# Optimization experiments

Measured on AMD Instinct MI355X. Metric: run time of the kernel, lower is better.

The kernel has to match this reference:

```python
import jax, jax.numpy as jnp
import numpy as np

S_LEN, T_LEN, BATCH, HID = 32, 32, 64, 512


def setup_inputs() -> dict:
    key = jax.random.key(0)
    ks = jax.random.split(key, 5)
    H = HID
    sc = lambda n: 1.0 / np.sqrt(n)
    return {
        "source": jax.random.normal(ks[0], (S_LEN, BATCH, H), jnp.float32),
        "target": jax.random.normal(ks[1], (T_LEN, BATCH, H), jnp.float32),
        # H2h Dense: concat(s_h, t_h) [B, 2H] -> [B, H], linear
        "W_H2h": (jax.random.normal(ks[2], (2 * H, H), jnp.float32) * sc(2 * H)),
        "b_H2h": jnp.zeros((H,), jnp.float32),
        # shared LSTMCell weights (Keras gate order i, f, g, o)
        "W_kernel": (jax.random.normal(ks[3], (H, 4 * H), jnp.float32) * sc(H)),
        "W_rec": (jax.random.normal(ks[4], (H, 4 * H), jnp.float32) * sc(H)),
        "b_lstm": jnp.zeros((4 * H,), jnp.float32),
    }


def _lstm_cell(x, h, c, Wk, Wr, b):
    # Keras LSTMCell math, gate order i, f, g(candidate), o
    z = x @ Wk + h @ Wr + b  # [B, 4H]
    i, f, g, o = jnp.split(z, 4, axis=-1)
    c2 = jax.nn.sigmoid(f) * c + jax.nn.sigmoid(i) * jnp.tanh(g)
    h2 = jax.nn.sigmoid(o) * jnp.tanh(c2)
    return h2, c2


def reference(source, target, W_H2h, b_H2h, W_kernel, W_rec, b_lstm):
    # source: [S, B, H] (time-major), target: [T, B, H]
    T, B, H = target.shape

    def inner(s_state, t_slice):
        # s_state carried along the target axis; t_slice is target cell j state
        s_step, s_h, s_m = s_state
        t_step, t_h, t_m = t_slice
        hmid = jnp.concatenate([s_h, t_h], axis=1) @ W_H2h + b_H2h  # [B, H]
        ns_h, ns_m = _lstm_cell(s_step, hmid, s_m, W_kernel, W_rec, b_lstm)
        nt_h, nt_m = _lstm_cell(t_step, hmid, t_m, W_kernel, W_rec, b_lstm)
        # step arrays get overwritten with the new hidden state
        return (ns_h, ns_h, ns_m), (nt_h, nt_h, nt_m)

    def outer(t_arrays, s_in):
        # fresh source state per outer step i: step = source[i], h = m = 0
        z = jnp.zeros_like(s_in)
        (s_step_f, _, _), t_new = jax.lax.scan(inner, (s_in, z, z), t_arrays)
        return t_new, s_step_f

    zeros = jnp.zeros((T, B, H), source.dtype)
    t_final, source_out = jax.lax.scan(outer, (target, zeros, zeros), source)
    return source_out, t_final[0]
```

## Files before the change

### kernel.cpp

```cpp
#include <hip/hip_runtime.h>

#define BLK 256

typedef __bf16 bf16;
typedef __bf16 bf16x8 __attribute__((ext_vector_type(8)));
typedef float f32x4 __attribute__((ext_vector_type(4)));

__device__ __forceinline__ float sigm(float x) { return 1.f / (1.f + __expf(-x)); }
__device__ __forceinline__ float tanh_(float x) {
    x = fminf(fmaxf(x, -15.f), 15.f);
    float e = __expf(2.f * x);
    return (e - 1.f) / (e + 1.f);
}

__device__ __forceinline__ void gl2lds(const bf16* g, bf16* l) {
    __builtin_amdgcn_global_load_lds((const __attribute__((address_space(1))) void*)g,
                                     (__attribute__((address_space(3))) void*)l, 16, 0, 0);
}

__global__ __launch_bounds__(256) void k_prep(
    const float* __restrict__ src, const float* __restrict__ tgt,
    const float* __restrict__ WH, const float* __restrict__ bH,
    const float* __restrict__ Wk, const float* __restrict__ Wr,
    const float* __restrict__ bl,
    bf16* __restrict__ srcb, bf16* __restrict__ tgtb,
    bf16* __restrict__ WHhi, bf16* __restrict__ WHlo,
    bf16* __restrict__ Wrhi, bf16* __restrict__ Wrlo,
    bf16* __restrict__ P2, float* __restrict__ bz) {
    __shared__ float tile[64][65];
    const int bid = blockIdx.x, t = threadIdx.x;
    if (bid < 512) {
        const float* in = (bid < 256) ? Wr : Wk;
        bf16* ohi = (bid < 256) ? Wrhi : P2;
        bf16* olo = (bid < 256) ? Wrlo : nullptr;
        const int b = bid & 255;
        const int tr = b >> 5, tc = b & 31;
#pragma unroll
        for (int q = 0; q < 16; q++) {
            int idx = q * 256 + t, lr = idx >> 6, lc = idx & 63;
            tile[lr][lc] = in[(size_t)(tr * 64 + lr) * 2048 + tc * 64 + lc];
        }
        __syncthreads();
#pragma unroll
        for (int q = 0; q < 16; q++) {
            int idx = q * 256 + t, lr = idx >> 6, lc = idx & 63;
            float v = tile[lc][lr];
            size_t o = (size_t)(tc * 64 + lr) * 512 + tr * 64 + lc;
            bf16 h = (bf16)v;
            ohi[o] = h;
            if (olo) olo[o] = (bf16)(v - (float)h);
        }
    } else if (bid < 520) {
        int c = (bid - 512) * 256 + t;
        float s = bl[c];
        for (int k = 0; k < 512; k++) s += bH[k] * Wr[(size_t)k * 2048 + c];
        bz[c] = s;
    } else {
        const int gt = (bid - 520) * 256 + t, NT = 504 * 256;
        for (int id = gt; id < 1048576; id += NT) srcb[id] = (bf16)src[id];
        for (int id = gt; id < 1048576; id += NT) tgtb[id] = (bf16)tgt[id];
        for (int id = gt; id < 524288; id += NT) {
            float v = WH[id];
            bf16 h = (bf16)v;
            WHhi[id] = h;
            WHlo[id] = (bf16)(v - (float)h);
        }
    }
}

__global__ __launch_bounds__(256, 4) void k_gemmP(
    const bf16* __restrict__ Wrhi, const bf16* __restrict__ Wrlo,
    const bf16* __restrict__ WHhi, const bf16* __restrict__ WHlo,
    bf16* __restrict__ P3, bf16* __restrict__ P4) {
    __shared__ __align__(16) bf16 At[64 * 64];
    __shared__ __align__(16) bf16 Bt[128 * 64];
    const int t = threadIdx.x, w = t >> 6, l = t & 63;
    const int m0 = (blockIdx.x >> 3) * 64, n0 = (blockIdx.x & 7) * 128;
    f32x4 acc[2][4] = {};
    const bf16* Aps[3] = {Wrhi, Wrlo, Wrhi};
    const bf16* Bps[3] = {WHhi, WHhi, WHlo};
    for (int ph = 0; ph < 3; ph++) {
        const bf16* Ap = Aps[ph] + (size_t)m0 * 512;
        const bf16* Bp = Bps[ph] + (size_t)n0 * 512;
        for (int kt = 0; kt < 8; kt++) {
            int k0 = kt * 64;
            __syncthreads();
#pragma unroll
            for (int q = 0; q < 2; q++) {
                int pp = q * 256 + t;
                int r = pp >> 3, c = (pp & 7) ^ (r & 7);
                gl2lds(Ap + (size_t)r * 512 + k0 + c * 8, &At[(q * 256 + w * 64) * 8]);
            }
#pragma unroll
            for (int q = 0; q < 4; q++) {
                int pp = q * 256 + t;
                int r = pp >> 3, c = (pp & 7) ^ (r & 7);
                gl2lds(Bp + (size_t)r * 512 + k0 + c * 8, &Bt[(q * 256 + w * 64) * 8]);
            }
            __syncthreads();
#pragma unroll
            for (int ks = 0; ks < 2; ks++) {
                int c = ks * 4 + (l >> 4);
                bf16x8 af[2], bb[4];
#pragma unroll
                for (int mt = 0; mt < 2; mt++) {
                    int r = (w >> 1) * 32 + mt * 16 + (l & 15);
                    af[mt] = *(const bf16x8*)&At[(r * 8 + (c ^ (r & 7))) * 8];
                }
#pragma unroll
                for (int g = 0; g < 4; g++) {
                    int r = g * 32 + (w & 1) * 16 + (l & 15);
                    bb[g] = *(const bf16x8*)&Bt[(r * 8 + (c ^ (r & 7))) * 8];
                }
#pragma unroll
                for (int mt = 0; mt < 2; mt++)
#pragma unroll
                    for (int g = 0; g < 4; g++)
                        acc[mt][g] = __builtin_amdgcn_mfma_f32_16x16x32_bf16(
                            af[mt], bb[g], acc[mt][g], 0, 0, 0);
            }
        }
    }
    const bool hihalf = (n0 >= 512);
#pragma unroll
    for (int mt = 0; mt < 2; mt++) {
#pragma unroll
        for (int g = 0; g < 4; g++) {
            int np = n0 + g * 32 + (w & 1) * 16 + (l & 15);
#pragma unroll
            for (int r = 0; r < 4; r++) {
                int c = m0 + (w >> 1) * 32 + mt * 16 + ((l >> 4) << 2) + r;
                float v = acc[mt][g][r];
                if (!hihalf) P4[(size_t)c * 512 + np] = (bf16)v;
                else P3[(size_t)c * 512 + (np - 512)] = (bf16)v;
            }
        }
    }
}

__global__ __launch_bounds__(256, 2) void k_diag4(
    int d, int i_lo,
    const bf16* __restrict__ srcb, const bf16* __restrict__ tgtb,
    const bf16* __restrict__ P2, const bf16* __restrict__ P3,
    const bf16* __restrict__ P4,
    const float* __restrict__ bz,
    const bf16* __restrict__ shR, bf16* __restrict__ shW,
    const bf16* __restrict__ thR, bf16* __restrict__ thW,
    float* __restrict__ sc, float* __restrict__ tc,
    float* __restrict__ out) {
    __shared__ __align__(16) bf16 As[64 * 64];
    __shared__ __align__(16) bf16 At2[64 * 64];
    __shared__ __align__(16) bf16 Bk[128 * 64];
    __shared__ __align__(16) bf16 Bs[128 * 64];
    __shared__ __align__(16) bf16 Bt[128 * 64];
    const int t = threadIdx.x, w = t >> 6, l = t & 63;
    const int cell = blockIdx.x >> 4, ch0 = (blockIdx.x & 15) << 5;
    const int i = i_lo + cell, j = d - i;
    const size_t stI = (size_t)i * 32768, stJ = (size_t)j * 32768;

    const bf16* Asrc = (j == 0 ? srcb : shR) + stI;
    const bf16* Atsrc = (i == 0 ? tgtb : thR) + stJ;
    const bool uS = (j > 0);
    const bool uT = (i > 0);

    f32x4 accS[2][4] = {};
    f32x4 accT[2][4] = {};
    f32x4 accU[2][4] = {};

#pragma unroll 1
    for (int kt = 0; kt < 8; kt++) {
        int k0 = kt * 64;
        __syncthreads();
#pragma unroll
        for (int q = 0; q < 2; q++) {
            int pp = q * 256 + t;
            int r = pp >> 3, c = (pp & 7) ^ (r & 7);
            gl2lds(Asrc + (size_t)r * 512 + k0 + c * 8, &As[(q * 256 + w * 64) * 8]);
        }
#pragma unroll
        for (int q = 0; q < 2; q++) {
            int pp = q * 256 + t;
            int r = pp >> 3, c = (pp & 7) ^ (r & 7);
            gl2lds(Atsrc + (size_t)r * 512 + k0 + c * 8, &At2[(q * 256 + w * 64) * 8]);
        }
#pragma unroll
        for (int q = 0; q < 4; q++) {
            int pp = q * 256 + t;
            int r = pp >> 3, c = (pp & 7) ^ (r & 7);
            size_t grow = (size_t)((r >> 5) * 512 + ch0 + (r & 31));
            gl2lds(P2 + grow * 512 + k0 + c * 8, &Bk[(q * 256 + w * 64) * 8]);
        }
        if (uS) {
#pragma unroll
            for (int q = 0; q < 4; q++) {
                int pp = q * 256 + t;
                int r = pp >> 3, c = (pp & 7) ^ (r & 7);
                size_t grow = (size_t)((r >> 5) * 512 + ch0 + (r & 31));
                gl2lds(P4 + grow * 512 + k0 + c * 8, &Bs[(q * 256 + w * 64) * 8]);
            }
        }
        if (uT) {
#pragma unroll
            for (int q = 0; q < 4; q++) {
                int pp = q * 256 + t;
                int r = pp >> 3, c = (pp & 7) ^ (r & 7);
                size_t grow = (size_t)((r >> 5) * 512 + ch0 + (r & 31));
                gl2lds(P3 + grow * 512 + k0 + c * 8, &Bt[(q * 256 + w * 64) * 8]);
            }
        }
        __syncthreads();
#pragma unroll
        for (int ks = 0; ks < 2; ks++) {
            int cq = ks * 4 + (l >> 4);
            bf16x8 aS[2], aT[2], bb[4];
#pragma unroll
            for (int mt = 0; mt < 2; mt++) {
                int r = (w >> 1) * 32 + mt * 16 + (l & 15);
                int cc = (r * 8 + (cq ^ (r & 7))) * 8;
                aS[mt] = *(const bf16x8*)&As[cc];
                aT[mt] = *(const bf16x8*)&At2[cc];
            }
#pragma unroll
            for (int g = 0; g < 4; g++) {
                int r = g * 32 + (w & 1) * 16 + (l & 15);
                bb[g] = *(const bf16x8*)&Bk[(r * 8 + (cq ^ (r & 7))) * 8];
            }
#pragma unroll
            for (int mt = 0; mt < 2; mt++)
#pragma unroll
                for (int g = 0; g < 4; g++) {
                    accS[mt][g] = __builtin_amdgcn_mfma_f32_16x16x32_bf16(
                        aS[mt], bb[g], accS[mt][g], 0, 0, 0);
                    accT[mt][g] = __builtin_amdgcn_mfma_f32_16x16x32_bf16(
                        aT[mt], bb[g], accT[mt][g], 0, 0, 0);
                }
            if (uS) {
#pragma unroll
                for (int g = 0; g < 4; g++) {
                    int r = g * 32 + (w & 1) * 16 + (l & 15);
                    bb[g] = *(const bf16x8*)&Bs[(r * 8 + (cq ^ (r & 7))) * 8];
                }
#pragma unroll
                for (int mt = 0; mt < 2; mt++)
#pragma unroll
                    for (int g = 0; g < 4; g++)
                        accU[mt][g] = __builtin_amdgcn_mfma_f32_16x16x32_bf16(
                            aS[mt], bb[g], accU[mt][g], 0, 0, 0);
            }
            if (uT) {
#pragma unroll
                for (int g = 0; g < 4; g++) {
                    int r = g * 32 + (w & 1) * 16 + (l & 15);
                    bb[g] = *(const bf16x8*)&Bt[(r * 8 + (cq ^ (r & 7))) * 8];
                }
#pragma unroll
                for (int mt = 0; mt < 2; mt++)
#pragma unroll
                    for (int g = 0; g < 4; g++)
                        accU[mt][g] = __builtin_amdgcn_mfma_f32_16x16x32_bf16(
                            aT[mt], bb[g], accU[mt][g], 0, 0, 0);
            }
        }
    }

    const int h = ch0 + (w & 1) * 16 + (l & 15);
    float bzv[4];
#pragma unroll
    for (int g = 0; g < 4; g++) bzv[g] = bz[g * 512 + h];
#pragma unroll
    for (int mt = 0; mt < 2; mt++) {
#pragma unroll
        for (int r = 0; r < 4; r++) {
            int b = (w >> 1) * 32 + mt * 16 + ((l >> 4) << 2) + r;
            float u0 = accU[mt][0][r], u1 = accU[mt][1][r];
            float u2 = accU[mt][2][r], u3 = accU[mt][3][r];
            {
                float zi = accS[mt][0][r] + u0 + bzv[0];
                float zf = accS[mt][1][r] + u1 + bzv[1];
                float zg = accS[mt][2][r] + u2 + bzv[2];
                float zo = accS[mt][3][r] + u3 + bzv[3];
                size_t off = stI + (size_t)b * 512 + h;
                float cold = uS ? sc[off] : 0.f;
                float c2 = sigm(zf) * cold + sigm(zi) * tanh_(zg);
                float h2 = sigm(zo) * tanh_(c2);
                sc[off] = c2;
                shW[off] = (bf16)h2;
                if (j == 31) out[off] = h2;
            }
            {
                float zi = accT[mt][0][r] + u0 + bzv[0];
                float zf = accT[mt][1][r] + u1 + bzv[1];
                float zg = accT[mt][2][r] + u2 + bzv[2];
                float zo = accT[mt][3][r] + u3 + bzv[3];
                size_t off = stJ + (size_t)b * 512 + h;
                float cold = uT ? tc[off] : 0.f;
                float c2 = sigm(zf) * cold + sigm(zi) * tanh_(zg);
                float h2 = sigm(zo) * tanh_(c2);
                tc[off] = c2;
                thW[off] = (bf16)h2;
                if (i == 31) out[1048576 + off] = h2;
            }
        }
    }
}


extern "C" void kernel_launch(void* const* d_in, const int* in_sizes, int n_in,
                              void* d_out, int out_size, void* d_ws, size_t ws_size,
                              hipStream_t stream) {
    char* w = (char*)d_ws;
    const size_t MB = 1u << 20;
    const float* src = (const float*)d_in[0];
    const float* tgt = (const float*)d_in[1];
    const float* WH = (const float*)d_in[2];
    const float* bH = (const float*)d_in[3];
    const float* Wk = (const float*)d_in[4];
    const float* Wr = (const float*)d_in[5];
    const float* bl = (const float*)d_in[6];
    float* out = (float*)d_out;

    bf16* srcb = (bf16*)(w + 0 * MB);
    bf16* tgtb = (bf16*)(w + 2 * MB);
    bf16* WHhi = (bf16*)(w + 4 * MB);
    bf16* WHlo = (bf16*)(w + 5 * MB);
    bf16* Wrhi = (bf16*)(w + 6 * MB);
    bf16* Wrlo = (bf16*)(w + 8 * MB);
    bf16* P2 = (bf16*)(w + 12 * MB);
    bf16* P3 = (bf16*)(w + 14 * MB);
    bf16* P4 = (bf16*)(w + 16 * MB);
    float* bz = (float*)(w + 20 * MB);
    bf16* sh = (bf16*)(w + 21 * MB);
    bf16* th = (bf16*)(w + 25 * MB);
    float* sc = (float*)(w + 29 * MB);
    float* tc = (float*)(w + 33 * MB);

    k_prep<<<1024, BLK, 0, stream>>>(src, tgt, WH, bH, Wk, Wr, bl, srcb, tgtb,
                                     WHhi, WHlo, Wrhi, Wrlo, P2, bz);
    k_gemmP<<<256, BLK, 0, stream>>>(Wrhi, Wrlo, WHhi, WHlo, P3, P4);

    for (int d = 0; d < 63; d++) {
        int i_lo = d > 31 ? d - 31 : 0;
        int i_hi = d < 31 ? d : 31;
        int Kd = i_hi - i_lo + 1;
        const bf16* shR = sh + (size_t)(d & 1) * 1048576;
        bf16* shW = sh + (size_t)((d + 1) & 1) * 1048576;
        const bf16* thR = th + (size_t)(d & 1) * 1048576;
        bf16* thW = th + (size_t)((d + 1) & 1) * 1048576;
        k_diag4<<<Kd * 16, BLK, 0, stream>>>(d, i_lo, srcb, tgtb, P2, P3, P4,
                                             bz, shR, shW, thR, thW, sc, tc, out);
    }
}
```

Before: 1.460 ms.

## Pair two wavefront cells per 512-thread block with double-buffered LDS staging

```diff
diff --git a/kernel.cpp b/kernel.cpp
--- a/kernel.cpp
+++ b/kernel.cpp
@@ -138,8 +138,8 @@
     }
 }
 
-__global__ __launch_bounds__(256, 2) void k_diag4(
-    int d, int i_lo,
+__global__ __launch_bounds__(512, 2) void k_diag5(
+    int d, int i_lo, int Kd,
     const bf16* __restrict__ srcb, const bf16* __restrict__ tgtb,
     const bf16* __restrict__ P2, const bf16* __restrict__ P3,
     const bf16* __restrict__ P4,
@@ -148,82 +148,69 @@
     const bf16* __restrict__ thR, bf16* __restrict__ thW,
     float* __restrict__ sc, float* __restrict__ tc,
     float* __restrict__ out) {
-    __shared__ __align__(16) bf16 As[64 * 64];
-    __shared__ __align__(16) bf16 At2[64 * 64];
-    __shared__ __align__(16) bf16 Bk[128 * 64];
-    __shared__ __align__(16) bf16 Bs[128 * 64];
-    __shared__ __align__(16) bf16 Bt[128 * 64];
+    __shared__ __align__(16) bf16 AL[2][4 * 4096];
+    __shared__ __align__(16) bf16 BL[2][3 * 8192];
     const int t = threadIdx.x, w = t >> 6, l = t & 63;
-    const int cell = blockIdx.x >> 4, ch0 = (blockIdx.x & 15) << 5;
-    const int i = i_lo + cell, j = d - i;
+    const int q = w >> 2, ww = w & 3;
+    const int pair = blockIdx.x >> 4, ch0 = (blockIdx.x & 15) << 5;
+    const int cell0 = pair * 2;
+    const bool valid = (cell0 + q) < Kd;
+    const int myCell = valid ? cell0 + q : cell0;
+    const int i = i_lo + myCell, j = d - i;
+    const bool uS = (j > 0), uT = (i > 0);
     const size_t stI = (size_t)i * 32768, stJ = (size_t)j * 32768;
 
-    const bf16* Asrc = (j == 0 ? srcb : shR) + stI;
-    const bf16* Atsrc = (i == 0 ? tgtb : thR) + stJ;
-    const bool uS = (j > 0);
-    const bool uT = (i > 0);
+    const int c1 = (cell0 + 1 < Kd) ? cell0 + 1 : cell0;
+    const int i0 = i_lo + cell0, j0 = d - i0;
+    const int i1 = i_lo + c1, j1 = d - i1;
+    const bf16* A0s = (j0 == 0 ? srcb : shR) + (size_t)i0 * 32768;
+    const bf16* A0t = (i0 == 0 ? tgtb : thR) + (size_t)j0 * 32768;
+    const bf16* A1s = (j1 == 0 ? srcb : shR) + (size_t)i1 * 32768;
+    const bf16* A1t = (i1 == 0 ? tgtb : thR) + (size_t)j1 * 32768;
 
     f32x4 accS[2][4] = {};
     f32x4 accT[2][4] = {};
     f32x4 accU[2][4] = {};
 
-#pragma unroll 1
-    for (int kt = 0; kt < 8; kt++) {
-        int k0 = kt * 64;
-        __syncthreads();
-#pragma unroll
-        for (int q = 0; q < 2; q++) {
-            int pp = q * 256 + t;
-            int r = pp >> 3, c = (pp & 7) ^ (r & 7);
-            gl2lds(Asrc + (size_t)r * 512 + k0 + c * 8, &As[(q * 256 + w * 64) * 8]);
-        }
-#pragma unroll
-        for (int q = 0; q < 2; q++) {
-            int pp = q * 256 + t;
-            int r = pp >> 3, c = (pp & 7) ^ (r & 7);
-            gl2lds(Atsrc + (size_t)r * 512 + k0 + c * 8, &At2[(q * 256 + w * 64) * 8]);
-        }
-#pragma unroll
-        for (int q = 0; q < 4; q++) {
-            int pp = q * 256 + t;
+    auto STAGE = [&](int bf, int k0) {
+        bf16* Ab = &AL[bf][0];
+        {
+            int r = t >> 3, c = (t & 7) ^ (r & 7);
+            size_t so = (size_t)r * 512 + k0 + c * 8;
+            gl2lds(A0s + so, Ab + (0 * 512 + w * 64) * 8);
+            gl2lds(A0t + so, Ab + (1 * 512 + w * 64) * 8);
+            gl2lds(A1s + so, Ab + (2 * 512 + w * 64) * 8);
+            gl2lds(A1t + so, Ab + (3 * 512 + w * 64) * 8);
+        }
+        bf16* Bb = &BL[bf][0];
+#pragma unroll
+        for (int qq = 0; qq < 6; qq++) {
+            int pp = (qq & 1) * 512 + t;
             int r = pp >> 3, c = (pp & 7) ^ (r & 7);
             size_t grow = (size_t)((r >> 5) * 512 + ch0 + (r & 31));
-            gl2lds(P2 + grow * 512 + k0 + c * 8, &Bk[(q * 256 + w * 64) * 8]);
-        }
-        if (uS) {
-#pragma unroll
-            for (int q = 0; q < 4; q++) {
-                int pp = q * 256 + t;
-                int r = pp >> 3, c = (pp & 7) ^ (r & 7);
-                size_t grow = (size_t)((r >> 5) * 512 + ch0 + (r & 31));
-                gl2lds(P4 + grow * 512 + k0 + c * 8, &Bs[(q * 256 + w * 64) * 8]);
-            }
-        }
-        if (uT) {
-#pragma unroll
-            for (int q = 0; q < 4; q++) {
-                int pp = q * 256 + t;
-                int r = pp >> 3, c = (pp & 7) ^ (r & 7);
-                size_t grow = (size_t)((r >> 5) * 512 + ch0 + (r & 31));
-                gl2lds(P3 + grow * 512 + k0 + c * 8, &Bt[(q * 256 + w * 64) * 8]);
-            }
-        }
-        __syncthreads();
+            const bf16* M = (qq < 2) ? P2 : (qq < 4) ? P4 : P3;
+            gl2lds(M + grow * 512 + k0 + c * 8, Bb + (qq * 512 + w * 64) * 8);
+        }
+    };
+
+    auto COMPUTE = [&](int bf) {
+        const bf16* Ab = &AL[bf][0];
+        const bf16* Bb = &BL[bf][0];
 #pragma unroll
         for (int ks = 0; ks < 2; ks++) {
             int cq = ks * 4 + (l >> 4);
             bf16x8 aS[2], aT[2], bb[4];
 #pragma unroll
             for (int mt = 0; mt < 2; mt++) {
-                int r = (w >> 1) * 32 + mt * 16 + (l & 15);
-                int cc = (r * 8 + (cq ^ (r & 7))) * 8;
-                aS[mt] = *(const bf16x8*)&As[cc];
-                aT[mt] = *(const bf16x8*)&At2[cc];
+                int r = (ww >> 1) * 32 + mt * 16 + (l & 15);
+                int co = (r * 8 + (cq ^ (r & 7))) * 8;
+                aS[mt] = *(const bf16x8*)&Ab[(q * 2) * 4096 + co];
+                aT[mt] = *(const bf16x8*)&Ab[(q * 2 + 1) * 4096 + co];
             }
 #pragma unroll
             for (int g = 0; g < 4; g++) {
-                int r = g * 32 + (w & 1) * 16 + (l & 15);
-                bb[g] = *(const bf16x8*)&Bk[(r * 8 + (cq ^ (r & 7))) * 8];
+                int r = g * 32 + (ww & 1) * 16 + (l & 15);
+                bb[g] = *(const bf16x8*)&Bb[(r * 8 + (cq ^ (r & 7))) * 8];
             }
 #pragma unroll
             for (int mt = 0; mt < 2; mt++)
@@ -237,8 +224,8 @@
             if (uS) {
 #pragma unroll
                 for (int g = 0; g < 4; g++) {
-                    int r = g * 32 + (w & 1) * 16 + (l & 15);
-                    bb[g] = *(const bf16x8*)&Bs[(r * 8 + (cq ^ (r & 7))) * 8];
+                    int r = g * 32 + (ww & 1) * 16 + (l & 15);
+                    bb[g] = *(const bf16x8*)&Bb[8192 + (r * 8 + (cq ^ (r & 7))) * 8];
                 }
 #pragma unroll
                 for (int mt = 0; mt < 2; mt++)
@@ -250,8 +237,8 @@
             if (uT) {
 #pragma unroll
                 for (int g = 0; g < 4; g++) {
-                    int r = g * 32 + (w & 1) * 16 + (l & 15);
-                    bb[g] = *(const bf16x8*)&Bt[(r * 8 + (cq ^ (r & 7))) * 8];
+                    int r = g * 32 + (ww & 1) * 16 + (l & 15);
+                    bb[g] = *(const bf16x8*)&Bb[16384 + (r * 8 + (cq ^ (r & 7))) * 8];
                 }
 #pragma unroll
                 for (int mt = 0; mt < 2; mt++)
@@ -261,9 +248,22 @@
                             aT[mt], bb[g], accU[mt][g], 0, 0, 0);
             }
         }
-    }
-
-    const int h = ch0 + (w & 1) * 16 + (l & 15);
+    };
+
+    STAGE(0, 0);
+    __syncthreads();
+    int bf = 0;
+#pragma unroll 1
+    for (int kt = 0; kt < 8; kt++) {
+        if (kt < 7) STAGE(bf ^ 1, (kt + 1) * 64);
+        COMPUTE(bf);
+        __syncthreads();
+        bf ^= 1;
+    }
+
+    if (!valid) return;
+
+    const int h = ch0 + (ww & 1) * 16 + (l & 15);
     float bzv[4];
 #pragma unroll
     for (int g = 0; g < 4; g++) bzv[g] = bz[g * 512 + h];
@@ -271,7 +271,7 @@
     for (int mt = 0; mt < 2; mt++) {
 #pragma unroll
         for (int r = 0; r < 4; r++) {
-            int b = (w >> 1) * 32 + mt * 16 + ((l >> 4) << 2) + r;
+            int b = (ww >> 1) * 32 + mt * 16 + ((l >> 4) << 2) + r;
             float u0 = accU[mt][0][r], u1 = accU[mt][1][r];
             float u2 = accU[mt][2][r], u3 = accU[mt][3][r];
             {
@@ -342,11 +342,12 @@
         int i_lo = d > 31 ? d - 31 : 0;
         int i_hi = d < 31 ? d : 31;
         int Kd = i_hi - i_lo + 1;
+        int nPairs = (Kd + 1) >> 1;
         const bf16* shR = sh + (size_t)(d & 1) * 1048576;
         bf16* shW = sh + (size_t)((d + 1) & 1) * 1048576;
         const bf16* thR = th + (size_t)(d & 1) * 1048576;
         bf16* thW = th + (size_t)((d + 1) & 1) * 1048576;
-        k_diag4<<<Kd * 16, BLK, 0, stream>>>(d, i_lo, srcb, tgtb, P2, P3, P4,
-                                             bz, shR, shW, thR, thW, sc, tc, out);
-    }
-}
+        k_diag5<<<nPairs * 16, 512, 0, stream>>>(d, i_lo, Kd, srcb, tgtb, P2, P3, P4,
+                                                 bz, shR, shW, thR, thW, sc, tc, out);
+    }
+}
```

Measured after the change: 1.705 ms. +16.7%, slower.

## Fold kernel weights into recurrent products and split diagonal cells by side

Applied to the files above, without the earlier changes.

```diff
diff --git a/kernel.cpp b/kernel.cpp
--- a/kernel.cpp
+++ b/kernel.cpp
@@ -71,7 +71,9 @@
 __global__ __launch_bounds__(256, 4) void k_gemmP(
     const bf16* __restrict__ Wrhi, const bf16* __restrict__ Wrlo,
     const bf16* __restrict__ WHhi, const bf16* __restrict__ WHlo,
-    bf16* __restrict__ P3, bf16* __restrict__ P4) {
+    const float* __restrict__ Wk,
+    bf16* __restrict__ P1, bf16* __restrict__ P3,
+    bf16* __restrict__ P4, bf16* __restrict__ P5) {
     __shared__ __align__(16) bf16 At[64 * 64];
     __shared__ __align__(16) bf16 Bt[128 * 64];
     const int t = threadIdx.x, w = t >> 6, l = t & 63;
@@ -131,123 +133,84 @@
             for (int r = 0; r < 4; r++) {
                 int c = m0 + (w >> 1) * 32 + mt * 16 + ((l >> 4) << 2) + r;
                 float v = acc[mt][g][r];
-                if (!hihalf) P4[(size_t)c * 512 + np] = (bf16)v;
-                else P3[(size_t)c * 512 + (np - 512)] = (bf16)v;
-            }
-        }
-    }
-}
-
-__global__ __launch_bounds__(256, 2) void k_diag4(
+                if (!hihalf) {
+                    P4[(size_t)c * 512 + np] = (bf16)v;
+                    P1[(size_t)c * 512 + np] = (bf16)(v + Wk[(size_t)np * 2048 + c]);
+                } else {
+                    int kk = np - 512;
+                    P3[(size_t)c * 512 + kk] = (bf16)v;
+                    P5[(size_t)c * 512 + kk] = (bf16)(v + Wk[(size_t)kk * 2048 + c]);
+                }
+            }
+        }
+    }
+}
+
+__global__ __launch_bounds__(256, 4) void k_diag6(
     int d, int i_lo,
     const bf16* __restrict__ srcb, const bf16* __restrict__ tgtb,
-    const bf16* __restrict__ P2, const bf16* __restrict__ P3,
-    const bf16* __restrict__ P4,
+    const bf16* __restrict__ P1, const bf16* __restrict__ P2,
+    const bf16* __restrict__ P3, const bf16* __restrict__ P4,
+    const bf16* __restrict__ P5,
     const float* __restrict__ bz,
     const bf16* __restrict__ shR, bf16* __restrict__ shW,
     const bf16* __restrict__ thR, bf16* __restrict__ thW,
     float* __restrict__ sc, float* __restrict__ tc,
     float* __restrict__ out) {
-    __shared__ __align__(16) bf16 As[64 * 64];
-    __shared__ __align__(16) bf16 At2[64 * 64];
-    __shared__ __align__(16) bf16 Bk[128 * 64];
-    __shared__ __align__(16) bf16 Bs[128 * 64];
+    __shared__ __align__(16) bf16 At[64 * 64];
     __shared__ __align__(16) bf16 Bt[128 * 64];
     const int t = threadIdx.x, w = t >> 6, l = t & 63;
-    const int cell = blockIdx.x >> 4, ch0 = (blockIdx.x & 15) << 5;
+    const int cell = blockIdx.x >> 5, sub = blockIdx.x & 31;
+    const int side = sub >> 4, ch0 = (sub & 15) << 5;
     const int i = i_lo + cell, j = d - i;
     const size_t stI = (size_t)i * 32768, stJ = (size_t)j * 32768;
 
-    const bf16* Asrc = (j == 0 ? srcb : shR) + stI;
-    const bf16* Atsrc = (i == 0 ? tgtb : thR) + stJ;
-    const bool uS = (j > 0);
-    const bool uT = (i > 0);
-
-    f32x4 accS[2][4] = {};
-    f32x4 accT[2][4] = {};
-    f32x4 accU[2][4] = {};
-
+    const bf16* Ah[2];
+    const bf16* Wh[2];
+    int nh = 0;
+    if (side == 0) {
+        Ah[nh] = (j == 0 ? srcb : shR) + stI;
+        Wh[nh] = (j == 0 ? P2 : P1);
+        nh++;
+        if (i > 0) { Ah[nh] = thR + stJ; Wh[nh] = P3; nh++; }
+    } else {
+        if (j > 0) { Ah[nh] = shR + stI; Wh[nh] = P4; nh++; }
+        Ah[nh] = (i == 0 ? tgtb : thR) + stJ;
+        Wh[nh] = (i == 0 ? P2 : P5);
+        nh++;
+    }
+
+    f32x4 acc[2][4] = {};
+    for (int hh = 0; hh < nh; hh++) {
+        const bf16* Ap = Ah[hh];
+        const bf16* Wp = Wh[hh];
 #pragma unroll 1
-    for (int kt = 0; kt < 8; kt++) {
-        int k0 = kt * 64;
-        __syncthreads();
-#pragma unroll
-        for (int q = 0; q < 2; q++) {
-            int pp = q * 256 + t;
-            int r = pp >> 3, c = (pp & 7) ^ (r & 7);
-            gl2lds(Asrc + (size_t)r * 512 + k0 + c * 8, &As[(q * 256 + w * 64) * 8]);
-        }
-#pragma unroll
-        for (int q = 0; q < 2; q++) {
-            int pp = q * 256 + t;
-            int r = pp >> 3, c = (pp & 7) ^ (r & 7);
-            gl2lds(Atsrc + (size_t)r * 512 + k0 + c * 8, &At2[(q * 256 + w * 64) * 8]);
-        }
-#pragma unroll
-        for (int q = 0; q < 4; q++) {
-            int pp = q * 256 + t;
-            int r = pp >> 3, c = (pp & 7) ^ (r & 7);
-            size_t grow = (size_t)((r >> 5) * 512 + ch0 + (r & 31));
-            gl2lds(P2 + grow * 512 + k0 + c * 8, &Bk[(q * 256 + w * 64) * 8]);
-        }
-        if (uS) {
+        for (int kt = 0; kt < 8; kt++) {
+            int k0 = kt * 64;
+            __syncthreads();
+#pragma unroll
+            for (int q = 0; q < 2; q++) {
+                int pp = q * 256 + t;
+                int r = pp >> 3, c = (pp & 7) ^ (r & 7);
+                gl2lds(Ap + (size_t)r * 512 + k0 + c * 8, &At[(q * 256 + w * 64) * 8]);
+            }
 #pragma unroll
             for (int q = 0; q < 4; q++) {
                 int pp = q * 256 + t;
                 int r = pp >> 3, c = (pp & 7) ^ (r & 7);
                 size_t grow = (size_t)((r >> 5) * 512 + ch0 + (r & 31));
-                gl2lds(P4 + grow * 512 + k0 + c * 8, &Bs[(q * 256 + w * 64) * 8]);
-            }
-        }
-        if (uT) {
-#pragma unroll
-            for (int q = 0; q < 4; q++) {
-                int pp = q * 256 + t;
-                int r = pp >> 3, c = (pp & 7) ^ (r & 7);
-                size_t grow = (size_t)((r >> 5) * 512 + ch0 + (r & 31));
-                gl2lds(P3 + grow * 512 + k0 + c * 8, &Bt[(q * 256 + w * 64) * 8]);
-            }
-        }
-        __syncthreads();
-#pragma unroll
-        for (int ks = 0; ks < 2; ks++) {
-            int cq = ks * 4 + (l >> 4);
-            bf16x8 aS[2], aT[2], bb[4];
-#pragma unroll
-            for (int mt = 0; mt < 2; mt++) {
-                int r = (w >> 1) * 32 + mt * 16 + (l & 15);
-                int cc = (r * 8 + (cq ^ (r & 7))) * 8;
-                aS[mt] = *(const bf16x8*)&As[cc];
-                aT[mt] = *(const bf16x8*)&At2[cc];
-            }
-#pragma unroll
-            for (int g = 0; g < 4; g++) {
-                int r = g * 32 + (w & 1) * 16 + (l & 15);
-                bb[g] = *(const bf16x8*)&Bk[(r * 8 + (cq ^ (r & 7))) * 8];
-            }
-#pragma unroll
-            for (int mt = 0; mt < 2; mt++)
-#pragma unroll
-                for (int g = 0; g < 4; g++) {
-                    accS[mt][g] = __builtin_amdgcn_mfma_f32_16x16x32_bf16(
-                        aS[mt], bb[g], accS[mt][g], 0, 0, 0);
-                    accT[mt][g] = __builtin_amdgcn_mfma_f32_16x16x32_bf16(
-                        aT[mt], bb[g], accT[mt][g], 0, 0, 0);
-                }
-            if (uS) {
-#pragma unroll
-                for (int g = 0; g < 4; g++) {
-                    int r = g * 32 + (w & 1) * 16 + (l & 15);
-                    bb[g] = *(const bf16x8*)&Bs[(r * 8 + (cq ^ (r & 7))) * 8];
-                }
-#pragma unroll
-                for (int mt = 0; mt < 2; mt++)
-#pragma unroll
-                    for (int g = 0; g < 4; g++)
-                        accU[mt][g] = __builtin_amdgcn_mfma_f32_16x16x32_bf16(
-                            aS[mt], bb[g], accU[mt][g], 0, 0, 0);
-            }
-            if (uT) {
+                gl2lds(Wp + grow * 512 + k0 + c * 8, &Bt[(q * 256 + w * 64) * 8]);
+            }
+            __syncthreads();
+#pragma unroll
+            for (int ks = 0; ks < 2; ks++) {
+                int cq = ks * 4 + (l >> 4);
+                bf16x8 af[2], bb[4];
+#pragma unroll
+                for (int mt = 0; mt < 2; mt++) {
+                    int r = (w >> 1) * 32 + mt * 16 + (l & 15);
+                    af[mt] = *(const bf16x8*)&At[(r * 8 + (cq ^ (r & 7))) * 8];
+                }
 #pragma unroll
                 for (int g = 0; g < 4; g++) {
                     int r = g * 32 + (w & 1) * 16 + (l & 15);
@@ -257,8 +220,8 @@
                 for (int mt = 0; mt < 2; mt++)
 #pragma unroll
                     for (int g = 0; g < 4; g++)
-                        accU[mt][g] = __builtin_amdgcn_mfma_f32_16x16x32_bf16(
-                            aT[mt], bb[g], accU[mt][g], 0, 0, 0);
+                        acc[mt][g] = __builtin_amdgcn_mfma_f32_16x16x32_bf16(
+                            af[mt], bb[g], acc[mt][g], 0, 0, 0);
             }
         }
     }
@@ -272,28 +235,21 @@
 #pragma unroll
         for (int r = 0; r < 4; r++) {
             int b = (w >> 1) * 32 + mt * 16 + ((l >> 4) << 2) + r;
-            float u0 = accU[mt][0][r], u1 = accU[mt][1][r];
-            float u2 = accU[mt][2][r], u3 = accU[mt][3][r];
-            {
-                float zi = accS[mt][0][r] + u0 + bzv[0];
-                float zf = accS[mt][1][r] + u1 + bzv[1];
-                float zg = accS[mt][2][r] + u2 + bzv[2];
-                float zo = accS[mt][3][r] + u3 + bzv[3];
+            float zi = acc[mt][0][r] + bzv[0];
+            float zf = acc[mt][1][r] + bzv[1];
+            float zg = acc[mt][2][r] + bzv[2];
+            float zo = acc[mt][3][r] + bzv[3];
+            if (side == 0) {
                 size_t off = stI + (size_t)b * 512 + h;
-                float cold = uS ? sc[off] : 0.f;
+                float cold = (j == 0) ? 0.f : sc[off];
                 float c2 = sigm(zf) * cold + sigm(zi) * tanh_(zg);
                 float h2 = sigm(zo) * tanh_(c2);
                 sc[off] = c2;
                 shW[off] = (bf16)h2;
                 if (j == 31) out[off] = h2;
-            }
-            {
-                float zi = accT[mt][0][r] + u0 + bzv[0];
-                float zf = accT[mt][1][r] + u1 + bzv[1];
-                float zg = accT[mt][2][r] + u2 + bzv[2];
-                float zo = accT[mt][3][r] + u3 + bzv[3];
+            } else {
                 size_t off = stJ + (size_t)b * 512 + h;
-                float cold = uT ? tc[off] : 0.f;
+                float cold = (i == 0) ? 0.f : tc[off];
                 float c2 = sigm(zf) * cold + sigm(zi) * tanh_(zg);
                 float h2 = sigm(zo) * tanh_(c2);
                 tc[off] = c2;
@@ -325,9 +281,11 @@
     bf16* WHlo = (bf16*)(w + 5 * MB);
     bf16* Wrhi = (bf16*)(w + 6 * MB);
     bf16* Wrlo = (bf16*)(w + 8 * MB);
+    bf16* P1 = (bf16*)(w + 10 * MB);
     bf16* P2 = (bf16*)(w + 12 * MB);
     bf16* P3 = (bf16*)(w + 14 * MB);
     bf16* P4 = (bf16*)(w + 16 * MB);
+    bf16* P5 = (bf16*)(w + 18 * MB);
     float* bz = (float*)(w + 20 * MB);
     bf16* sh = (bf16*)(w + 21 * MB);
     bf16* th = (bf16*)(w + 25 * MB);
@@ -336,7 +294,7 @@
 
     k_prep<<<1024, BLK, 0, stream>>>(src, tgt, WH, bH, Wk, Wr, bl, srcb, tgtb,
                                      WHhi, WHlo, Wrhi, Wrlo, P2, bz);
-    k_gemmP<<<256, BLK, 0, stream>>>(Wrhi, Wrlo, WHhi, WHlo, P3, P4);
+    k_gemmP<<<256, BLK, 0, stream>>>(Wrhi, Wrlo, WHhi, WHlo, Wk, P1, P3, P4, P5);
 
     for (int d = 0; d < 63; d++) {
         int i_lo = d > 31 ? d - 31 : 0;
@@ -346,7 +304,7 @@
         bf16* shW = sh + (size_t)((d + 1) & 1) * 1048576;
         const bf16* thR = th + (size_t)(d & 1) * 1048576;
         bf16* thW = th + (size_t)((d + 1) & 1) * 1048576;
-        k_diag4<<<Kd * 16, BLK, 0, stream>>>(d, i_lo, srcb, tgtb, P2, P3, P4,
+        k_diag6<<<Kd * 32, BLK, 0, stream>>>(d, i_lo, srcb, tgtb, P1, P2, P3, P4, P5,
                                              bz, shR, shW, thR, thW, sc, tc, out);
     }
 }
```

Result: faster. 1.425 ms (-2.4%).

## Halve K-tile to cut LDS, raise occupancy, and remap blocks across XCDs

Applied to the files above, without the earlier changes.

```diff
diff --git a/kernel.cpp b/kernel.cpp
--- a/kernel.cpp
+++ b/kernel.cpp
@@ -138,8 +138,8 @@
     }
 }
 
-__global__ __launch_bounds__(256, 2) void k_diag4(
-    int d, int i_lo,
+__global__ __launch_bounds__(256, 3) void k_diag7(
+    int d, int i_lo, int Kd,
     const bf16* __restrict__ srcb, const bf16* __restrict__ tgtb,
     const bf16* __restrict__ P2, const bf16* __restrict__ P3,
     const bf16* __restrict__ P4,
@@ -148,118 +148,97 @@
     const bf16* __restrict__ thR, bf16* __restrict__ thW,
     float* __restrict__ sc, float* __restrict__ tc,
     float* __restrict__ out) {
-    __shared__ __align__(16) bf16 As[64 * 64];
-    __shared__ __align__(16) bf16 At2[64 * 64];
-    __shared__ __align__(16) bf16 Bk[128 * 64];
-    __shared__ __align__(16) bf16 Bs[128 * 64];
-    __shared__ __align__(16) bf16 Bt[128 * 64];
+    __shared__ __align__(16) bf16 As[64 * 32];
+    __shared__ __align__(16) bf16 At2[64 * 32];
+    __shared__ __align__(16) bf16 Bk[128 * 32];
+    __shared__ __align__(16) bf16 Bs[128 * 32];
+    __shared__ __align__(16) bf16 Bt[128 * 32];
     const int t = threadIdx.x, w = t >> 6, l = t & 63;
-    const int cell = blockIdx.x >> 4, ch0 = (blockIdx.x & 15) << 5;
+    const int bid = blockIdx.x;
+    const int xcd = bid & 7, idx = bid >> 3;
+    const int ch0 = (xcd * 2 + (idx & 1)) << 5;
+    const int cell = idx >> 1;
     const int i = i_lo + cell, j = d - i;
+    const bool uS = (j > 0), uT = (i > 0);
     const size_t stI = (size_t)i * 32768, stJ = (size_t)j * 32768;
 
     const bf16* Asrc = (j == 0 ? srcb : shR) + stI;
     const bf16* Atsrc = (i == 0 ? tgtb : thR) + stJ;
-    const bool uS = (j > 0);
-    const bool uT = (i > 0);
 
     f32x4 accS[2][4] = {};
     f32x4 accT[2][4] = {};
     f32x4 accU[2][4] = {};
 
 #pragma unroll 1
-    for (int kt = 0; kt < 8; kt++) {
-        int k0 = kt * 64;
+    for (int kt = 0; kt < 16; kt++) {
+        const int k0 = kt * 32;
         __syncthreads();
+        {
+            int rA = t >> 2, cA = (t & 3) ^ (rA & 3);
+            size_t soA = (size_t)rA * 512 + k0 + cA * 8;
+            gl2lds(Asrc + soA, As + w * 512);
+            gl2lds(Atsrc + soA, At2 + w * 512);
+        }
 #pragma unroll
         for (int q = 0; q < 2; q++) {
             int pp = q * 256 + t;
-            int r = pp >> 3, c = (pp & 7) ^ (r & 7);
-            gl2lds(Asrc + (size_t)r * 512 + k0 + c * 8, &As[(q * 256 + w * 64) * 8]);
-        }
-#pragma unroll
-        for (int q = 0; q < 2; q++) {
-            int pp = q * 256 + t;
-            int r = pp >> 3, c = (pp & 7) ^ (r & 7);
-            gl2lds(Atsrc + (size_t)r * 512 + k0 + c * 8, &At2[(q * 256 + w * 64) * 8]);
-        }
-#pragma unroll
-        for (int q = 0; q < 4; q++) {
-            int pp = q * 256 + t;
-            int r = pp >> 3, c = (pp & 7) ^ (r & 7);
-            size_t grow = (size_t)((r >> 5) * 512 + ch0 + (r & 31));
-            gl2lds(P2 + grow * 512 + k0 + c * 8, &Bk[(q * 256 + w * 64) * 8]);
-        }
+            int r = pp >> 2, c = (pp & 3) ^ (r & 3);
+            size_t so = (size_t)((r >> 5) * 512 + ch0 + (r & 31)) * 512 + k0 + c * 8;
+            int dsto = (q * 256 + w * 64) * 8;
+            gl2lds(P2 + so, Bk + dsto);
+            if (uS) gl2lds(P4 + so, Bs + dsto);
+            if (uT) gl2lds(P3 + so, Bt + dsto);
+        }
+        __syncthreads();
+
+        const int cq = l >> 4;
+        bf16x8 aS[2], aT[2], bb[4];
+#pragma unroll
+        for (int mt = 0; mt < 2; mt++) {
+            int r = (w >> 1) * 32 + mt * 16 + (l & 15);
+            int co = (r * 4 + (cq ^ (r & 3))) * 8;
+            aS[mt] = *(const bf16x8*)&As[co];
+            aT[mt] = *(const bf16x8*)&At2[co];
+        }
+#pragma unroll
+        for (int g = 0; g < 4; g++) {
+            int r = g * 32 + (w & 1) * 16 + (l & 15);
+            bb[g] = *(const bf16x8*)&Bk[(r * 4 + (cq ^ (r & 3))) * 8];
+        }
+#pragma unroll
+        for (int mt = 0; mt < 2; mt++)
+#pragma unroll
+            for (int g = 0; g < 4; g++) {
+                accS[mt][g] = __builtin_amdgcn_mfma_f32_16x16x32_bf16(
+                    aS[mt], bb[g], accS[mt][g], 0, 0, 0);
+                accT[mt][g] = __builtin_amdgcn_mfma_f32_16x16x32_bf16(
+                    aT[mt], bb[g], accT[mt][g], 0, 0, 0);
+            }
         if (uS) {
-#pragma unroll
-            for (int q = 0; q < 4; q++) {
-                int pp = q * 256 + t;
-                int r = pp >> 3, c = (pp & 7) ^ (r & 7);
-                size_t grow = (size_t)((r >> 5) * 512 + ch0 + (r & 31));
-                gl2lds(P4 + grow * 512 + k0 + c * 8, &Bs[(q * 256 + w * 64) * 8]);
-            }
-        }
-        if (uT) {
-#pragma unroll
-            for (int q = 0; q < 4; q++) {
-                int pp = q * 256 + t;
-                int r = pp >> 3, c = (pp & 7) ^ (r & 7);
-                size_t grow = (size_t)((r >> 5) * 512 + ch0 + (r & 31));
-                gl2lds(P3 + grow * 512 + k0 + c * 8, &Bt[(q * 256 + w * 64) * 8]);
-            }
-        }
-        __syncthreads();
-#pragma unroll
-        for (int ks = 0; ks < 2; ks++) {
-            int cq = ks * 4 + (l >> 4);
-            bf16x8 aS[2], aT[2], bb[4];
-#pragma unroll
-            for (int mt = 0; mt < 2; mt++) {
-                int r = (w >> 1) * 32 + mt * 16 + (l & 15);
-                int cc = (r * 8 + (cq ^ (r & 7))) * 8;
-                aS[mt] = *(const bf16x8*)&As[cc];
-                aT[mt] = *(const bf16x8*)&At2[cc];
-            }
 #pragma unroll
             for (int g = 0; g < 4; g++) {
                 int r = g * 32 + (w & 1) * 16 + (l & 15);
-                bb[g] = *(const bf16x8*)&Bk[(r * 8 + (cq ^ (r & 7))) * 8];
+                bb[g] = *(const bf16x8*)&Bs[(r * 4 + (cq ^ (r & 3))) * 8];
             }
 #pragma unroll
             for (int mt = 0; mt < 2; mt++)
 #pragma unroll
-                for (int g = 0; g < 4; g++) {
-                    accS[mt][g] = __builtin_amdgcn_mfma_f32_16x16x32_bf16(
-                        aS[mt], bb[g], accS[mt][g], 0, 0, 0);
-                    accT[mt][g] = __builtin_amdgcn_mfma_f32_16x16x32_bf16(
-                        aT[mt], bb[g], accT[mt][g], 0, 0, 0);
-                }
-            if (uS) {
-#pragma unroll
-                for (int g = 0; g < 4; g++) {
-                    int r = g * 32 + (w & 1) * 16 + (l & 15);
-                    bb[g] = *(const bf16x8*)&Bs[(r * 8 + (cq ^ (r & 7))) * 8];
-                }
-#pragma unroll
-                for (int mt = 0; mt < 2; mt++)
-#pragma unroll
-                    for (int g = 0; g < 4; g++)
-                        accU[mt][g] = __builtin_amdgcn_mfma_f32_16x16x32_bf16(
-                            aS[mt], bb[g], accU[mt][g], 0, 0, 0);
-            }
-            if (uT) {
-#pragma unroll
-                for (int g = 0; g < 4; g++) {
-                    int r = g * 32 + (w & 1) * 16 + (l & 15);
-                    bb[g] = *(const bf16x8*)&Bt[(r * 8 + (cq ^ (r & 7))) * 8];
-                }
-#pragma unroll
-                for (int mt = 0; mt < 2; mt++)
-#pragma unroll
-                    for (int g = 0; g < 4; g++)
-                        accU[mt][g] = __builtin_amdgcn_mfma_f32_16x16x32_bf16(
-                            aT[mt], bb[g], accU[mt][g], 0, 0, 0);
-            }
+                for (int g = 0; g < 4; g++)
+                    accU[mt][g] = __builtin_amdgcn_mfma_f32_16x16x32_bf16(
+                        aS[mt], bb[g], accU[mt][g], 0, 0, 0);
+        }
+        if (uT) {
+#pragma unroll
+            for (int g = 0; g < 4; g++) {
+                int r = g * 32 + (w & 1) * 16 + (l & 15);
+                bb[g] = *(const bf16x8*)&Bt[(r * 4 + (cq ^ (r & 3))) * 8];
+            }
+#pragma unroll
+            for (int mt = 0; mt < 2; mt++)
+#pragma unroll
+                for (int g = 0; g < 4; g++)
+                    accU[mt][g] = __builtin_amdgcn_mfma_f32_16x16x32_bf16(
+                        aT[mt], bb[g], accU[mt][g], 0, 0, 0);
         }
     }
 
@@ -346,7 +325,7 @@
         bf16* shW = sh + (size_t)((d + 1) & 1) * 1048576;
         const bf16* thR = th + (size_t)(d & 1) * 1048576;
         bf16* thW = th + (size_t)((d + 1) & 1) * 1048576;
-        k_diag4<<<Kd * 16, BLK, 0, stream>>>(d, i_lo, srcb, tgtb, P2, P3, P4,
+        k_diag7<<<Kd * 16, BLK, 0, stream>>>(d, i_lo, Kd, srcb, tgtb, P2, P3, P4,
                                              bz, shR, shW, thR, thW, sc, tc, out);
     }
 }
```

Result: slower. 1.681 ms (+15.1%).
